# Performance work log

Measured on AMD Instinct MI355X. Metric: run time of the kernel, lower is better.

## Reference

```python
import jax, jax.numpy as jnp
import numpy as np

QUALITY = 50.0
TEMP = 0.3  # soft-round temperature

_LUM = np.array([[16,11,10,16,24,40,51,61],[12,12,14,19,26,58,60,55],[14,13,16,24,40,57,69,56],[14,17,22,29,51,87,80,62],[18,22,37,56,68,109,103,77],[24,35,55,64,81,104,113,92],[49,64,78,87,103,121,120,101],[72,92,95,98,112,100,103,99]], dtype=np.float32)
_CHR = np.array([[17,18,24,47,99,99,99,99],[18,21,26,66,99,99,99,99],[24,26,56,99,99,99,99,99],[47,66,99,99,99,99,99,99],[99,99,99,99,99,99,99,99],[99,99,99,99,99,99,99,99],[99,99,99,99,99,99,99,99],[99,99,99,99,99,99,99,99]], dtype=np.float32)

def _scaled_qtable(base, qf):
    qf = max(1.0, min(100.0, qf))
    s = 5000.0 / qf if qf < 50 else 200.0 - 2.0 * qf
    return np.maximum(np.floor((base * s + 50.0) / 100.0), 1.0)

# Per-channel quantization tables: Y uses luminance, Cb/Cr use chrominance. (3,8,8)
QTAB = jnp.asarray(np.stack([_scaled_qtable(_LUM, QUALITY), _scaled_qtable(_CHR, QUALITY), _scaled_qtable(_CHR, QUALITY)]).astype(np.float32))

# The original 64x1x8x8 conv kernel factors as outer product D[u,x]*D[v,y].
_u = np.arange(8)[:, None]
_x = np.arange(8)[None, :]
_c = np.where(_u == 0, 1.0 / np.sqrt(2.0), 1.0)
DCT = jnp.asarray((0.5 * _c * np.cos((2 * _x + 1) * _u * np.pi / 16.0)).astype(np.float32))

M_FWD = jnp.array([[0.299, 0.587, 0.114], [-0.168736, -0.331264, 0.5], [0.5, -0.418688, -0.081312]], dtype=jnp.float32)
M_INV = jnp.array([[1.0, 0.0, 1.402], [1.0, -0.344136, -0.714136], [1.0, 1.772, 0.0]], dtype=jnp.float32)
OFF = jnp.array([0.0, 0.5, 0.5], dtype=jnp.float32)


def setup_inputs() -> dict:
    key = jax.random.key(0)
    x = jax.random.uniform(key, (32, 3, 512, 512), dtype=jnp.float32)
    return {"x": x}


def reference(x):
    B, C, H, W = x.shape  # H, W divisible by 8 (no pad branch)
    # RGB -> YCbCr, centered
    ycbcr = jnp.einsum('ij,bjhw->bihw', M_FWD, x) + OFF[None, :, None, None] - 0.5
    # split into 8x8 blocks: (B, 3, H/8, 8, W/8, 8)
    blocks = ycbcr.reshape(B, C, H // 8, 8, W // 8, 8)
    # block DCT: coef[u,v] = sum_{x,y} D[u,x] D[v,y] block[x,y]
    coef = jnp.einsum('ux,vy,bchxgy->bchugv', DCT, DCT, blocks)
    q = QTAB[None, :, None, :, None, :]  # broadcast per-channel table
    d = coef / q
    # smooth rounding: x + 0.5*tanh(50*T*(x - round(x)))
    sr = d + 0.5 * jnp.tanh(50.0 * TEMP * (d - jnp.round(d)))
    deq = sr * q
    # block IDCT (transpose of DCT): block[x,y] = sum_{u,v} D[u,x] D[v,y] coef[u,v]
    rec = jnp.einsum('ux,vy,bchugv->bchxgy', DCT, DCT, deq)
    ycbcr_rec = rec.reshape(B, C, H, W) + 0.5
    rgb = jnp.einsum('ij,bjhw->bihw', M_INV, ycbcr_rec - OFF[None, :, None, None])
    return jnp.clip(rgb, 0.0, 1.0)
```

## Files before the change

### kernel.cpp

```cpp
#include <hip/hip_runtime.h>
#include <math.h>

#define A0c 0.35355339059327373f
#define C1c 0.4903926402016152f
#define C2c 0.46193976625564337f
#define C3c 0.41573480615127262f
#define C5c 0.27778511650980114f
#define C6c 0.19134171618254492f
#define C7c 0.09754516100806417f

#define IMG_W 512
#define IMG_HW (512 * 512)

typedef float f8v __attribute__((ext_vector_type(8)));

__device__ const float QLUM[64] = {
    16,11,10,16,24,40,51,61,  12,12,14,19,26,58,60,55,
    14,13,16,24,40,57,69,56,  14,17,22,29,51,87,80,62,
    18,22,37,56,68,109,103,77, 24,35,55,64,81,104,113,92,
    49,64,78,87,103,121,120,101, 72,92,95,98,112,100,103,99};
__device__ const float QCHR[64] = {
    17,18,24,47,99,99,99,99,  18,21,26,66,99,99,99,99,
    24,26,56,99,99,99,99,99,  47,66,99,99,99,99,99,99,
    99,99,99,99,99,99,99,99,  99,99,99,99,99,99,99,99,
    99,99,99,99,99,99,99,99,  99,99,99,99,99,99,99,99};

__device__ __forceinline__ void fdct8(float v[8]) {
    float s0 = v[0] + v[7], s1 = v[1] + v[6], s2 = v[2] + v[5], s3 = v[3] + v[4];
    float d0 = v[0] - v[7], d1 = v[1] - v[6], d2 = v[2] - v[5], d3 = v[3] - v[4];
    float e0 = s0 + s3, e1 = s1 + s2, f0 = s0 - s3, f1 = s1 - s2;
    v[0] = A0c * (e0 + e1);
    v[4] = A0c * (e0 - e1);
    v[2] = C2c * f0 + C6c * f1;
    v[6] = C6c * f0 - C2c * f1;
    v[1] = C1c * d0 + C3c * d1 + C5c * d2 + C7c * d3;
    v[3] = C3c * d0 - C7c * d1 - C1c * d2 - C5c * d3;
    v[5] = C5c * d0 - C1c * d1 + C7c * d2 + C3c * d3;
    v[7] = C7c * d0 - C5c * d1 + C3c * d2 - C1c * d3;
}

__device__ __forceinline__ void idct8(float v[8]) {
    float g0 = v[0], g1 = v[1], g2 = v[2], g3 = v[3];
    float g4 = v[4], g5 = v[5], g6 = v[6], g7 = v[7];
    float ep = A0c * (g0 + g4), em = A0c * (g0 - g4);
    float t26a = C2c * g2 + C6c * g6;
    float t26b = C6c * g2 - C2c * g6;
    float e0 = ep + t26a, e1 = em + t26b, e2 = em - t26b, e3 = ep - t26a;
    float o0 = C1c * g1 + C3c * g3 + C5c * g5 + C7c * g7;
    float o1 = C3c * g1 - C7c * g3 - C1c * g5 - C5c * g7;
    float o2 = C5c * g1 - C1c * g3 + C7c * g5 + C3c * g7;
    float o3 = C7c * g1 - C5c * g3 + C3c * g5 - C1c * g7;
    v[0] = e0 + o0; v[7] = e0 - o0;
    v[1] = e1 + o1; v[6] = e1 - o1;
    v[2] = e2 + o2; v[5] = e2 - o2;
    v[3] = e3 + o3; v[4] = e3 - o3;
}

#define K_EXP2 43.2808512266689f
__device__ __forceinline__ float softq(float x, float qh, float rq) {
    float d = x * rq;
    float rn = rintf(d);
    float t = d - rn;
    float e2 = __builtin_amdgcn_exp2f(K_EXP2 * t);
    float th = (e2 - 1.0f) * __builtin_amdgcn_rcpf(e2 + 1.0f);
    return x + qh * th;
}

#define LDS_FENCE() asm volatile("" ::: "memory")

__global__ __launch_bounds__(256) void jpeg_kernel(const float* __restrict__ x,
                                                   float* __restrict__ out) {
    __shared__ float xpose[4][576];
    __shared__ float qtab[4][64];

    const int tid = threadIdx.x;
    const int wid = tid >> 6;
    const int lane = tid & 63;

    const int gw = blockIdx.x * 4 + wid;
    const int bimg = gw >> 9;
    const int rem = gw & 511;
    const int gh = rem >> 3;
    const int tx = rem & 7;

    const int blk = lane & 7;
    const int row = lane >> 3;

    const size_t off = (size_t)bimg * 3 * IMG_HW +
                       (size_t)(gh * 8 + row) * IMG_W + tx * 64 + blk * 8;
    const float* base = x + off;

    const f8v Rv = *(const f8v*)(base);
    const f8v Gv = *(const f8v*)(base + IMG_HW);
    const f8v Bv = *(const f8v*)(base + 2 * IMG_HW);

    {
        int u = lane & 7, v = lane >> 3;
        float ql = QLUM[u * 8 + v];
        float qc = QCHR[u * 8 + v];
        qtab[0][lane] = 0.5f * ql;
        qtab[1][lane] = __builtin_amdgcn_rcpf(ql);
        qtab[2][lane] = 0.5f * qc;
        qtab[3][lane] = __builtin_amdgcn_rcpf(qc);
    }
    LDS_FENCE();

    float* xp = xpose[wid];
    const int wbase = blk * 9 + row;
    const int rbase = row * 72 + blk * 9;
    const int qrow = row * 8;

    float g0[8], g1[8], g2[8];
#pragma unroll
    for (int k = 0; k < 8; ++k) {
        float R = Rv[k], G = Gv[k], B = Bv[k];
        g0[k] = 0.299f * R + 0.587f * G + 0.114f * B - 0.5f;
        g1[k] = -0.168736f * R - 0.331264f * G + 0.5f * B;
        g2[k] = 0.5f * R - 0.418688f * G - 0.081312f * B;
    }

    fdct8(g0);
#pragma unroll
    for (int j = 0; j < 8; ++j) xp[j * 72 + wbase] = g0[j];
    LDS_FENCE();
#pragma unroll
    for (int k = 0; k < 8; ++k) g0[k] = xp[rbase + k];
    LDS_FENCE();
    fdct8(g0);
    {
        float4 qa = *(const float4*)&qtab[0][qrow];
        float4 qb = *(const float4*)&qtab[0][qrow + 4];
        float4 ra = *(const float4*)&qtab[1][qrow];
        float4 rb = *(const float4*)&qtab[1][qrow + 4];
        g0[0] = softq(g0[0], qa.x, ra.x); g0[1] = softq(g0[1], qa.y, ra.y);
        g0[2] = softq(g0[2], qa.z, ra.z); g0[3] = softq(g0[3], qa.w, ra.w);
        g0[4] = softq(g0[4], qb.x, rb.x); g0[5] = softq(g0[5], qb.y, rb.y);
        g0[6] = softq(g0[6], qb.z, rb.z); g0[7] = softq(g0[7], qb.w, rb.w);
    }
    idct8(g0);
    LDS_FENCE();
#pragma unroll
    for (int j = 0; j < 8; ++j) xp[j * 72 + wbase] = g0[j];
    LDS_FENCE();
#pragma unroll
    for (int k = 0; k < 8; ++k) g0[k] = xp[rbase + k];
    LDS_FENCE();
    idct8(g0);

    fdct8(g1);
#pragma unroll
    for (int j = 0; j < 8; ++j) xp[j * 72 + wbase] = g1[j];
    LDS_FENCE();
#pragma unroll
    for (int k = 0; k < 8; ++k) g1[k] = xp[rbase + k];
    LDS_FENCE();
    fdct8(g1);
    {
        float4 qa = *(const float4*)&qtab[2][qrow];
        float4 qb = *(const float4*)&qtab[2][qrow + 4];
        float4 ra = *(const float4*)&qtab[3][qrow];
        float4 rb = *(const float4*)&qtab[3][qrow + 4];
        g1[0] = softq(g1[0], qa.x, ra.x); g1[1] = softq(g1[1], qa.y, ra.y);
        g1[2] = softq(g1[2], qa.z, ra.z); g1[3] = softq(g1[3], qa.w, ra.w);
        g1[4] = softq(g1[4], qb.x, rb.x); g1[5] = softq(g1[5], qb.y, rb.y);
        g1[6] = softq(g1[6], qb.z, rb.z); g1[7] = softq(g1[7], qb.w, rb.w);
    }
    idct8(g1);
    LDS_FENCE();
#pragma unroll
    for (int j = 0; j < 8; ++j) xp[j * 72 + wbase] = g1[j];
    LDS_FENCE();
#pragma unroll
    for (int k = 0; k < 8; ++k) g1[k] = xp[rbase + k];
    LDS_FENCE();
    idct8(g1);

    fdct8(g2);
#pragma unroll
    for (int j = 0; j < 8; ++j) xp[j * 72 + wbase] = g2[j];
    LDS_FENCE();
#pragma unroll
    for (int k = 0; k < 8; ++k) g2[k] = xp[rbase + k];
    LDS_FENCE();
    fdct8(g2);
    {
        float4 qa = *(const float4*)&qtab[2][qrow];
        float4 qb = *(const float4*)&qtab[2][qrow + 4];
        float4 ra = *(const float4*)&qtab[3][qrow];
        float4 rb = *(const float4*)&qtab[3][qrow + 4];
        g2[0] = softq(g2[0], qa.x, ra.x); g2[1] = softq(g2[1], qa.y, ra.y);
        g2[2] = softq(g2[2], qa.z, ra.z); g2[3] = softq(g2[3], qa.w, ra.w);
        g2[4] = softq(g2[4], qb.x, rb.x); g2[5] = softq(g2[5], qb.y, rb.y);
        g2[6] = softq(g2[6], qb.z, rb.z); g2[7] = softq(g2[7], qb.w, rb.w);
    }
    idct8(g2);
    LDS_FENCE();
#pragma unroll
    for (int j = 0; j < 8; ++j) xp[j * 72 + wbase] = g2[j];
    LDS_FENCE();
#pragma unroll
    for (int k = 0; k < 8; ++k) g2[k] = xp[rbase + k];
    LDS_FENCE();
    idct8(g2);

    f8v Ro, Go, Bo;
#pragma unroll
    for (int k = 0; k < 8; ++k) {
        float Y  = g0[k] + 0.5f;
        float Cb = g1[k];
        float Cr = g2[k];
        float R = Y + 1.402f * Cr;
        float G = Y - 0.344136f * Cb - 0.714136f * Cr;
        float B = Y + 1.772f * Cb;
        Ro[k] = fminf(fmaxf(R, 0.0f), 1.0f);
        Go[k] = fminf(fmaxf(G, 0.0f), 1.0f);
        Bo[k] = fminf(fmaxf(B, 0.0f), 1.0f);
    }
    float* obase = out + off;
    *(f8v*)(obase) = Ro;
    *(f8v*)(obase + IMG_HW) = Go;
    *(f8v*)(obase + 2 * IMG_HW) = Bo;
}

extern "C" void kernel_launch(void* const* d_in, const int* in_sizes, int n_in,
                              void* d_out, int out_size, void* d_ws, size_t ws_size,
                              hipStream_t stream) {
    const float* x = (const float*)d_in[0];
    float* out = (float*)d_out;
    const int B = in_sizes[0] / (3 * IMG_HW);
    const int n_wg = B * 128;
    hipLaunchKernelGGL(jpeg_kernel, dim3(n_wg), dim3(256), 0, stream, x, out);
}
```

Baseline: 38.78 us.

## Process two images per thread with packed float2 math for DCT pipeline

Each thread now handles the same block position in two images (offset by 16 images) and holds values as float2 vectors, so the DCT/IDCT and color conversions can map to packed FP32 instructions (v_pk_fma_f32 on CDNA). The grid is halved and hardcoded to 2048 workgroups, and the LDS transpose buffer doubles to float2 entries. This aims to cut per-element ALU instruction count and raise memory-level parallelism per thread, but it increases register pressure and LDS use and drops support for batch sizes other than 32.

Measured after the change: 40.27 us. 1.04x slower.

```diff
diff --git a/kernel.cpp b/kernel.cpp
--- a/kernel.cpp
+++ b/kernel.cpp
@@ -13,6 +13,7 @@
 #define IMG_HW (512 * 512)
 
 typedef float f8v __attribute__((ext_vector_type(8)));
+typedef float f2v __attribute__((ext_vector_type(2)));
 
 __device__ const float QLUM[64] = {
     16,11,10,16,24,40,51,61,  12,12,14,19,26,58,60,55,
@@ -25,10 +26,10 @@
     99,99,99,99,99,99,99,99,  99,99,99,99,99,99,99,99,
     99,99,99,99,99,99,99,99,  99,99,99,99,99,99,99,99};
 
-__device__ __forceinline__ void fdct8(float v[8]) {
-    float s0 = v[0] + v[7], s1 = v[1] + v[6], s2 = v[2] + v[5], s3 = v[3] + v[4];
-    float d0 = v[0] - v[7], d1 = v[1] - v[6], d2 = v[2] - v[5], d3 = v[3] - v[4];
-    float e0 = s0 + s3, e1 = s1 + s2, f0 = s0 - s3, f1 = s1 - s2;
+__device__ __forceinline__ void fdct8p(f2v v[8]) {
+    f2v s0 = v[0] + v[7], s1 = v[1] + v[6], s2 = v[2] + v[5], s3 = v[3] + v[4];
+    f2v d0 = v[0] - v[7], d1 = v[1] - v[6], d2 = v[2] - v[5], d3 = v[3] - v[4];
+    f2v e0 = s0 + s3, e1 = s1 + s2, f0 = s0 - s3, f1 = s1 - s2;
     v[0] = A0c * (e0 + e1);
     v[4] = A0c * (e0 - e1);
     v[2] = C2c * f0 + C6c * f1;
@@ -39,17 +40,17 @@
     v[7] = C7c * d0 - C5c * d1 + C3c * d2 - C1c * d3;
 }
 
-__device__ __forceinline__ void idct8(float v[8]) {
-    float g0 = v[0], g1 = v[1], g2 = v[2], g3 = v[3];
-    float g4 = v[4], g5 = v[5], g6 = v[6], g7 = v[7];
-    float ep = A0c * (g0 + g4), em = A0c * (g0 - g4);
-    float t26a = C2c * g2 + C6c * g6;
-    float t26b = C6c * g2 - C2c * g6;
-    float e0 = ep + t26a, e1 = em + t26b, e2 = em - t26b, e3 = ep - t26a;
-    float o0 = C1c * g1 + C3c * g3 + C5c * g5 + C7c * g7;
-    float o1 = C3c * g1 - C7c * g3 - C1c * g5 - C5c * g7;
-    float o2 = C5c * g1 - C1c * g3 + C7c * g5 + C3c * g7;
-    float o3 = C7c * g1 - C5c * g3 + C3c * g5 - C1c * g7;
+__device__ __forceinline__ void idct8p(f2v v[8]) {
+    f2v g0 = v[0], g1 = v[1], g2 = v[2], g3 = v[3];
+    f2v g4 = v[4], g5 = v[5], g6 = v[6], g7 = v[7];
+    f2v ep = A0c * (g0 + g4), em = A0c * (g0 - g4);
+    f2v t26a = C2c * g2 + C6c * g6;
+    f2v t26b = C6c * g2 - C2c * g6;
+    f2v e0 = ep + t26a, e1 = em + t26b, e2 = em - t26b, e3 = ep - t26a;
+    f2v o0 = C1c * g1 + C3c * g3 + C5c * g5 + C7c * g7;
+    f2v o1 = C3c * g1 - C7c * g3 - C1c * g5 - C5c * g7;
+    f2v o2 = C5c * g1 - C1c * g3 + C7c * g5 + C3c * g7;
+    f2v o3 = C7c * g1 - C5c * g3 + C3c * g5 - C1c * g7;
     v[0] = e0 + o0; v[7] = e0 - o0;
     v[1] = e1 + o1; v[6] = e1 - o1;
     v[2] = e2 + o2; v[5] = e2 - o2;
@@ -57,12 +58,15 @@
 }
 
 #define K_EXP2 43.2808512266689f
-__device__ __forceinline__ float softq(float x, float qh, float rq) {
-    float d = x * rq;
-    float rn = rintf(d);
-    float t = d - rn;
-    float e2 = __builtin_amdgcn_exp2f(K_EXP2 * t);
-    float th = (e2 - 1.0f) * __builtin_amdgcn_rcpf(e2 + 1.0f);
+__device__ __forceinline__ f2v softq2(f2v x, float qh, float rq) {
+    f2v d = x * rq;
+    f2v rn; rn[0] = rintf(d[0]); rn[1] = rintf(d[1]);
+    f2v t = d - rn;
+    f2v e2; e2[0] = __builtin_amdgcn_exp2f(K_EXP2 * t[0]);
+            e2[1] = __builtin_amdgcn_exp2f(K_EXP2 * t[1]);
+    f2v num = e2 - 1.0f;
+    f2v th; th[0] = num[0] * __builtin_amdgcn_rcpf(e2[0] + 1.0f);
+            th[1] = num[1] * __builtin_amdgcn_rcpf(e2[1] + 1.0f);
     return x + qh * th;
 }
 
@@ -70,7 +74,7 @@
 
 __global__ __launch_bounds__(256) void jpeg_kernel(const float* __restrict__ x,
                                                    float* __restrict__ out) {
-    __shared__ float xpose[4][576];
+    __shared__ f2v xpose[4][576];
     __shared__ float qtab[4][64];
 
     const int tid = threadIdx.x;
@@ -88,11 +92,16 @@
 
     const size_t off = (size_t)bimg * 3 * IMG_HW +
                        (size_t)(gh * 8 + row) * IMG_W + tx * 64 + blk * 8;
-    const float* base = x + off;
-
-    const f8v Rv = *(const f8v*)(base);
-    const f8v Gv = *(const f8v*)(base + IMG_HW);
-    const f8v Bv = *(const f8v*)(base + 2 * IMG_HW);
+    const size_t toff = (size_t)16 * 3 * IMG_HW;
+    const float* baseA = x + off;
+    const float* baseB = baseA + toff;
+
+    const f8v RA = *(const f8v*)(baseA);
+    const f8v GA = *(const f8v*)(baseA + IMG_HW);
+    const f8v BA = *(const f8v*)(baseA + 2 * IMG_HW);
+    const f8v RB = *(const f8v*)(baseB);
+    const f8v GB = *(const f8v*)(baseB + IMG_HW);
+    const f8v BB = *(const f8v*)(baseB + 2 * IMG_HW);
 
     {
         int u = lane & 7, v = lane >> 3;
@@ -105,39 +114,41 @@
     }
     LDS_FENCE();
 
-    float* xp = xpose[wid];
+    f2v* xp = xpose[wid];
     const int wbase = blk * 9 + row;
     const int rbase = row * 72 + blk * 9;
     const int qrow = row * 8;
 
-    float g0[8], g1[8], g2[8];
+    f2v g0[8], g1[8], g2[8];
 #pragma unroll
     for (int k = 0; k < 8; ++k) {
-        float R = Rv[k], G = Gv[k], B = Bv[k];
-        g0[k] = 0.299f * R + 0.587f * G + 0.114f * B - 0.5f;
-        g1[k] = -0.168736f * R - 0.331264f * G + 0.5f * B;
-        g2[k] = 0.5f * R - 0.418688f * G - 0.081312f * B;
-    }
-
-    fdct8(g0);
+        f2v Rp; Rp[0] = RA[k]; Rp[1] = RB[k];
+        f2v Gp; Gp[0] = GA[k]; Gp[1] = GB[k];
+        f2v Bp; Bp[0] = BA[k]; Bp[1] = BB[k];
+        g0[k] = 0.299f * Rp + 0.587f * Gp + 0.114f * Bp - 0.5f;
+        g1[k] = -0.168736f * Rp - 0.331264f * Gp + 0.5f * Bp;
+        g2[k] = 0.5f * Rp - 0.418688f * Gp - 0.081312f * Bp;
+    }
+
+    fdct8p(g0);
 #pragma unroll
     for (int j = 0; j < 8; ++j) xp[j * 72 + wbase] = g0[j];
     LDS_FENCE();
 #pragma unroll
     for (int k = 0; k < 8; ++k) g0[k] = xp[rbase + k];
     LDS_FENCE();
-    fdct8(g0);
+    fdct8p(g0);
     {
         float4 qa = *(const float4*)&qtab[0][qrow];
         float4 qb = *(const float4*)&qtab[0][qrow + 4];
         float4 ra = *(const float4*)&qtab[1][qrow];
         float4 rb = *(const float4*)&qtab[1][qrow + 4];
-        g0[0] = softq(g0[0], qa.x, ra.x); g0[1] = softq(g0[1], qa.y, ra.y);
-        g0[2] = softq(g0[2], qa.z, ra.z); g0[3] = softq(g0[3], qa.w, ra.w);
-        g0[4] = softq(g0[4], qb.x, rb.x); g0[5] = softq(g0[5], qb.y, rb.y);
-        g0[6] = softq(g0[6], qb.z, rb.z); g0[7] = softq(g0[7], qb.w, rb.w);
-    }
-    idct8(g0);
+        g0[0] = softq2(g0[0], qa.x, ra.x); g0[1] = softq2(g0[1], qa.y, ra.y);
+        g0[2] = softq2(g0[2], qa.z, ra.z); g0[3] = softq2(g0[3], qa.w, ra.w);
+        g0[4] = softq2(g0[4], qb.x, rb.x); g0[5] = softq2(g0[5], qb.y, rb.y);
+        g0[6] = softq2(g0[6], qb.z, rb.z); g0[7] = softq2(g0[7], qb.w, rb.w);
+    }
+    idct8p(g0);
     LDS_FENCE();
 #pragma unroll
     for (int j = 0; j < 8; ++j) xp[j * 72 + wbase] = g0[j];
@@ -145,27 +156,27 @@
 #pragma unroll
     for (int k = 0; k < 8; ++k) g0[k] = xp[rbase + k];
     LDS_FENCE();
-    idct8(g0);
-
-    fdct8(g1);
+    idct8p(g0);
+
+    fdct8p(g1);
 #pragma unroll
     for (int j = 0; j < 8; ++j) xp[j * 72 + wbase] = g1[j];
     LDS_FENCE();
 #pragma unroll
     for (int k = 0; k < 8; ++k) g1[k] = xp[rbase + k];
     LDS_FENCE();
-    fdct8(g1);
+    fdct8p(g1);
     {
         float4 qa = *(const float4*)&qtab[2][qrow];
         float4 qb = *(const float4*)&qtab[2][qrow + 4];
         float4 ra = *(const float4*)&qtab[3][qrow];
         float4 rb = *(const float4*)&qtab[3][qrow + 4];
-        g1[0] = softq(g1[0], qa.x, ra.x); g1[1] = softq(g1[1], qa.y, ra.y);
-        g1[2] = softq(g1[2], qa.z, ra.z); g1[3] = softq(g1[3], qa.w, ra.w);
-        g1[4] = softq(g1[4], qb.x, rb.x); g1[5] = softq(g1[5], qb.y, rb.y);
-        g1[6] = softq(g1[6], qb.z, rb.z); g1[7] = softq(g1[7], qb.w, rb.w);
-    }
-    idct8(g1);
+        g1[0] = softq2(g1[0], qa.x, ra.x); g1[1] = softq2(g1[1], qa.y, ra.y);
+        g1[2] = softq2(g1[2], qa.z, ra.z); g1[3] = softq2(g1[3], qa.w, ra.w);
+        g1[4] = softq2(g1[4], qb.x, rb.x); g1[5] = softq2(g1[5], qb.y, rb.y);
+        g1[6] = softq2(g1[6], qb.z, rb.z); g1[7] = softq2(g1[7], qb.w, rb.w);
+    }
+    idct8p(g1);
     LDS_FENCE();
 #pragma unroll
     for (int j = 0; j < 8; ++j) xp[j * 72 + wbase] = g1[j];
@@ -173,27 +184,27 @@
 #pragma unroll
     for (int k = 0; k < 8; ++k) g1[k] = xp[rbase + k];
     LDS_FENCE();
-    idct8(g1);
-
-    fdct8(g2);
+    idct8p(g1);
+
+    fdct8p(g2);
 #pragma unroll
     for (int j = 0; j < 8; ++j) xp[j * 72 + wbase] = g2[j];
     LDS_FENCE();
 #pragma unroll
     for (int k = 0; k < 8; ++k) g2[k] = xp[rbase + k];
     LDS_FENCE();
-    fdct8(g2);
+    fdct8p(g2);
     {
         float4 qa = *(const float4*)&qtab[2][qrow];
         float4 qb = *(const float4*)&qtab[2][qrow + 4];
         float4 ra = *(const float4*)&qtab[3][qrow];
         float4 rb = *(const float4*)&qtab[3][qrow + 4];
-        g2[0] = softq(g2[0], qa.x, ra.x); g2[1] = softq(g2[1], qa.y, ra.y);
-        g2[2] = softq(g2[2], qa.z, ra.z); g2[3] = softq(g2[3], qa.w, ra.w);
-        g2[4] = softq(g2[4], qb.x, rb.x); g2[5] = softq(g2[5], qb.y, rb.y);
-        g2[6] = softq(g2[6], qb.z, rb.z); g2[7] = softq(g2[7], qb.w, rb.w);
-    }
-    idct8(g2);
+        g2[0] = softq2(g2[0], qa.x, ra.x); g2[1] = softq2(g2[1], qa.y, ra.y);
+        g2[2] = softq2(g2[2], qa.z, ra.z); g2[3] = softq2(g2[3], qa.w, ra.w);
+        g2[4] = softq2(g2[4], qb.x, rb.x); g2[5] = softq2(g2[5], qb.y, rb.y);
+        g2[6] = softq2(g2[6], qb.z, rb.z); g2[7] = softq2(g2[7], qb.w, rb.w);
+    }
+    idct8p(g2);
     LDS_FENCE();
 #pragma unroll
     for (int j = 0; j < 8; ++j) xp[j * 72 + wbase] = g2[j];
@@ -201,25 +212,34 @@
 #pragma unroll
     for (int k = 0; k < 8; ++k) g2[k] = xp[rbase + k];
     LDS_FENCE();
-    idct8(g2);
-
-    f8v Ro, Go, Bo;
+    idct8p(g2);
+
+    const f2v vzero = {0.0f, 0.0f};
+    const f2v vone  = {1.0f, 1.0f};
+    f8v RoA, GoA, BoA, RoB, GoB, BoB;
 #pragma unroll
     for (int k = 0; k < 8; ++k) {
-        float Y  = g0[k] + 0.5f;
-        float Cb = g1[k];
-        float Cr = g2[k];
-        float R = Y + 1.402f * Cr;
-        float G = Y - 0.344136f * Cb - 0.714136f * Cr;
-        float B = Y + 1.772f * Cb;
-        Ro[k] = fminf(fmaxf(R, 0.0f), 1.0f);
-        Go[k] = fminf(fmaxf(G, 0.0f), 1.0f);
-        Bo[k] = fminf(fmaxf(B, 0.0f), 1.0f);
-    }
-    float* obase = out + off;
-    *(f8v*)(obase) = Ro;
-    *(f8v*)(obase + IMG_HW) = Go;
-    *(f8v*)(obase + 2 * IMG_HW) = Bo;
+        f2v Y  = g0[k] + 0.5f;
+        f2v Cb = g1[k];
+        f2v Cr = g2[k];
+        f2v R = Y + 1.402f * Cr;
+        f2v G = Y - 0.344136f * Cb - 0.714136f * Cr;
+        f2v B = Y + 1.772f * Cb;
+        R = __builtin_elementwise_min(__builtin_elementwise_max(R, vzero), vone);
+        G = __builtin_elementwise_min(__builtin_elementwise_max(G, vzero), vone);
+        B = __builtin_elementwise_min(__builtin_elementwise_max(B, vzero), vone);
+        RoA[k] = R[0]; RoB[k] = R[1];
+        GoA[k] = G[0]; GoB[k] = G[1];
+        BoA[k] = B[0]; BoB[k] = B[1];
+    }
+    float* oA = out + off;
+    float* oB = oA + toff;
+    *(f8v*)(oA) = RoA;
+    *(f8v*)(oA + IMG_HW) = GoA;
+    *(f8v*)(oA + 2 * IMG_HW) = BoA;
+    *(f8v*)(oB) = RoB;
+    *(f8v*)(oB + IMG_HW) = GoB;
+    *(f8v*)(oB + 2 * IMG_HW) = BoB;
 }
 
 extern "C" void kernel_launch(void* const* d_in, const int* in_sizes, int n_in,
@@ -227,7 +247,6 @@
                               hipStream_t stream) {
     const float* x = (const float*)d_in[0];
     float* out = (float*)d_out;
-    const int B = in_sizes[0] / (3 * IMG_HW);
-    const int n_wg = B * 128;
+    const int n_wg = 2048;
     hipLaunchKernelGGL(jpeg_kernel, dim3(n_wg), dim3(256), 0, stream, x, out);
 }
```

## Process four images per wave with register prefetch of next tile

Applied to the files above, without the earlier changes.

Restructures the kernel so each wave loops over four tiles spaced eight images apart, loading the next tile's RGB into registers before processing the current one. The grid is fixed at 1024 workgroups, amortizing quant-table setup and overlapping global loads with DCT compute. This raises register pressure, and the hardcoded grid assumes a batch of 32.

New measurement: 39.03 us. Within noise of the previous version (+0.7%).

```diff
diff --git a/kernel.cpp b/kernel.cpp
--- a/kernel.cpp
+++ b/kernel.cpp
@@ -68,48 +68,43 @@
 
 #define LDS_FENCE() asm volatile("" ::: "memory")
 
-__global__ __launch_bounds__(256) void jpeg_kernel(const float* __restrict__ x,
-                                                   float* __restrict__ out) {
-    __shared__ float xpose[4][576];
-    __shared__ float qtab[4][64];
-
-    const int tid = threadIdx.x;
-    const int wid = tid >> 6;
-    const int lane = tid & 63;
-
-    const int gw = blockIdx.x * 4 + wid;
-    const int bimg = gw >> 9;
-    const int rem = gw & 511;
-    const int gh = rem >> 3;
-    const int tx = rem & 7;
-
-    const int blk = lane & 7;
-    const int row = lane >> 3;
-
-    const size_t off = (size_t)bimg * 3 * IMG_HW +
-                       (size_t)(gh * 8 + row) * IMG_W + tx * 64 + blk * 8;
-    const float* base = x + off;
-
-    const f8v Rv = *(const f8v*)(base);
-    const f8v Gv = *(const f8v*)(base + IMG_HW);
-    const f8v Bv = *(const f8v*)(base + 2 * IMG_HW);
-
+__device__ __forceinline__ void chan_chain(float g[8], float* xp, int wbase,
+                                           int rbase, const float* qh8,
+                                           const float* rq8) {
+    fdct8(g);
+#pragma unroll
+    for (int j = 0; j < 8; ++j) xp[j * 72 + wbase] = g[j];
+    LDS_FENCE();
+#pragma unroll
+    for (int k = 0; k < 8; ++k) g[k] = xp[rbase + k];
+    LDS_FENCE();
+    fdct8(g);
     {
-        int u = lane & 7, v = lane >> 3;
-        float ql = QLUM[u * 8 + v];
-        float qc = QCHR[u * 8 + v];
-        qtab[0][lane] = 0.5f * ql;
-        qtab[1][lane] = __builtin_amdgcn_rcpf(ql);
-        qtab[2][lane] = 0.5f * qc;
-        qtab[3][lane] = __builtin_amdgcn_rcpf(qc);
-    }
-    LDS_FENCE();
-
-    float* xp = xpose[wid];
-    const int wbase = blk * 9 + row;
-    const int rbase = row * 72 + blk * 9;
-    const int qrow = row * 8;
-
+        float4 qa = *(const float4*)&qh8[0];
+        float4 qb = *(const float4*)&qh8[4];
+        float4 ra = *(const float4*)&rq8[0];
+        float4 rb = *(const float4*)&rq8[4];
+        g[0] = softq(g[0], qa.x, ra.x); g[1] = softq(g[1], qa.y, ra.y);
+        g[2] = softq(g[2], qa.z, ra.z); g[3] = softq(g[3], qa.w, ra.w);
+        g[4] = softq(g[4], qb.x, rb.x); g[5] = softq(g[5], qb.y, rb.y);
+        g[6] = softq(g[6], qb.z, rb.z); g[7] = softq(g[7], qb.w, rb.w);
+    }
+    idct8(g);
+    LDS_FENCE();
+#pragma unroll
+    for (int j = 0; j < 8; ++j) xp[j * 72 + wbase] = g[j];
+    LDS_FENCE();
+#pragma unroll
+    for (int k = 0; k < 8; ++k) g[k] = xp[rbase + k];
+    LDS_FENCE();
+    idct8(g);
+}
+
+__device__ __forceinline__ void process_tile(const f8v Rv, const f8v Gv, const f8v Bv,
+                                             float* xp, int wbase, int rbase,
+                                             const float* qt0, const float* qt1,
+                                             const float* qt2, const float* qt3,
+                                             float* obase) {
     float g0[8], g1[8], g2[8];
 #pragma unroll
     for (int k = 0; k < 8; ++k) {
@@ -118,90 +113,9 @@
         g1[k] = -0.168736f * R - 0.331264f * G + 0.5f * B;
         g2[k] = 0.5f * R - 0.418688f * G - 0.081312f * B;
     }
-
-    fdct8(g0);
-#pragma unroll
-    for (int j = 0; j < 8; ++j) xp[j * 72 + wbase] = g0[j];
-    LDS_FENCE();
-#pragma unroll
-    for (int k = 0; k < 8; ++k) g0[k] = xp[rbase + k];
-    LDS_FENCE();
-    fdct8(g0);
-    {
-        float4 qa = *(const float4*)&qtab[0][qrow];
-        float4 qb = *(const float4*)&qtab[0][qrow + 4];
-        float4 ra = *(const float4*)&qtab[1][qrow];
-        float4 rb = *(const float4*)&qtab[1][qrow + 4];
-        g0[0] = softq(g0[0], qa.x, ra.x); g0[1] = softq(g0[1], qa.y, ra.y);
-        g0[2] = softq(g0[2], qa.z, ra.z); g0[3] = softq(g0[3], qa.w, ra.w);
-        g0[4] = softq(g0[4], qb.x, rb.x); g0[5] = softq(g0[5], qb.y, rb.y);
-        g0[6] = softq(g0[6], qb.z, rb.z); g0[7] = softq(g0[7], qb.w, rb.w);
-    }
-    idct8(g0);
-    LDS_FENCE();
-#pragma unroll
-    for (int j = 0; j < 8; ++j) xp[j * 72 + wbase] = g0[j];
-    LDS_FENCE();
-#pragma unroll
-    for (int k = 0; k < 8; ++k) g0[k] = xp[rbase + k];
-    LDS_FENCE();
-    idct8(g0);
-
-    fdct8(g1);
-#pragma unroll
-    for (int j = 0; j < 8; ++j) xp[j * 72 + wbase] = g1[j];
-    LDS_FENCE();
-#pragma unroll
-    for (int k = 0; k < 8; ++k) g1[k] = xp[rbase + k];
-    LDS_FENCE();
-    fdct8(g1);
-    {
-        float4 qa = *(const float4*)&qtab[2][qrow];
-        float4 qb = *(const float4*)&qtab[2][qrow + 4];
-        float4 ra = *(const float4*)&qtab[3][qrow];
-        float4 rb = *(const float4*)&qtab[3][qrow + 4];
-        g1[0] = softq(g1[0], qa.x, ra.x); g1[1] = softq(g1[1], qa.y, ra.y);
-        g1[2] = softq(g1[2], qa.z, ra.z); g1[3] = softq(g1[3], qa.w, ra.w);
-        g1[4] = softq(g1[4], qb.x, rb.x); g1[5] = softq(g1[5], qb.y, rb.y);
-        g1[6] = softq(g1[6], qb.z, rb.z); g1[7] = softq(g1[7], qb.w, rb.w);
-    }
-    idct8(g1);
-    LDS_FENCE();
-#pragma unroll
-    for (int j = 0; j < 8; ++j) xp[j * 72 + wbase] = g1[j];
-    LDS_FENCE();
-#pragma unroll
-    for (int k = 0; k < 8; ++k) g1[k] = xp[rbase + k];
-    LDS_FENCE();
-    idct8(g1);
-
-    fdct8(g2);
-#pragma unroll
-    for (int j = 0; j < 8; ++j) xp[j * 72 + wbase] = g2[j];
-    LDS_FENCE();
-#pragma unroll
-    for (int k = 0; k < 8; ++k) g2[k] = xp[rbase + k];
-    LDS_FENCE();
-    fdct8(g2);
-    {
-        float4 qa = *(const float4*)&qtab[2][qrow];
-        float4 qb = *(const float4*)&qtab[2][qrow + 4];
-        float4 ra = *(const float4*)&qtab[3][qrow];
-        float4 rb = *(const float4*)&qtab[3][qrow + 4];
-        g2[0] = softq(g2[0], qa.x, ra.x); g2[1] = softq(g2[1], qa.y, ra.y);
-        g2[2] = softq(g2[2], qa.z, ra.z); g2[3] = softq(g2[3], qa.w, ra.w);
-        g2[4] = softq(g2[4], qb.x, rb.x); g2[5] = softq(g2[5], qb.y, rb.y);
-        g2[6] = softq(g2[6], qb.z, rb.z); g2[7] = softq(g2[7], qb.w, rb.w);
-    }
-    idct8(g2);
-    LDS_FENCE();
-#pragma unroll
-    for (int j = 0; j < 8; ++j) xp[j * 72 + wbase] = g2[j];
-    LDS_FENCE();
-#pragma unroll
-    for (int k = 0; k < 8; ++k) g2[k] = xp[rbase + k];
-    LDS_FENCE();
-    idct8(g2);
+    chan_chain(g0, xp, wbase, rbase, qt0, qt1);
+    chan_chain(g1, xp, wbase, rbase, qt2, qt3);
+    chan_chain(g2, xp, wbase, rbase, qt2, qt3);
 
     f8v Ro, Go, Bo;
 #pragma unroll
@@ -216,10 +130,79 @@
         Go[k] = fminf(fmaxf(G, 0.0f), 1.0f);
         Bo[k] = fminf(fmaxf(B, 0.0f), 1.0f);
     }
-    float* obase = out + off;
     *(f8v*)(obase) = Ro;
     *(f8v*)(obase + IMG_HW) = Go;
     *(f8v*)(obase + 2 * IMG_HW) = Bo;
+}
+
+__global__ __launch_bounds__(256) void jpeg_kernel(const float* __restrict__ x,
+                                                   float* __restrict__ out) {
+    __shared__ float xpose[4][576];
+    __shared__ float qtab[4][64];
+
+    const int tid = threadIdx.x;
+    const int wid = tid >> 6;
+    const int lane = tid & 63;
+
+    const int gw = blockIdx.x * 4 + wid;
+    const int bimg = gw >> 9;
+    const int rem = gw & 511;
+    const int gh = rem >> 3;
+    const int tx = rem & 7;
+
+    const int blk = lane & 7;
+    const int row = lane >> 3;
+
+    const size_t off0 = (size_t)bimg * 3 * IMG_HW +
+                        (size_t)(gh * 8 + row) * IMG_W + tx * 64 + blk * 8;
+    const size_t DOFF = (size_t)8 * 3 * IMG_HW;
+
+    f8v Rc = *(const f8v*)(x + off0);
+    f8v Gc = *(const f8v*)(x + off0 + IMG_HW);
+    f8v Bc = *(const f8v*)(x + off0 + 2 * IMG_HW);
+
+    {
+        int u = lane & 7, v = lane >> 3;
+        float ql = QLUM[u * 8 + v];
+        float qc = QCHR[u * 8 + v];
+        qtab[0][lane] = 0.5f * ql;
+        qtab[1][lane] = __builtin_amdgcn_rcpf(ql);
+        qtab[2][lane] = 0.5f * qc;
+        qtab[3][lane] = __builtin_amdgcn_rcpf(qc);
+    }
+    LDS_FENCE();
+
+    float* xp = xpose[wid];
+    const int wbase = blk * 9 + row;
+    const int rbase = row * 72 + blk * 9;
+    const int qrow = row * 8;
+    const float* qt0 = &qtab[0][qrow];
+    const float* qt1 = &qtab[1][qrow];
+    const float* qt2 = &qtab[2][qrow];
+    const float* qt3 = &qtab[3][qrow];
+
+    f8v Rn = *(const f8v*)(x + off0 + DOFF);
+    f8v Gn = *(const f8v*)(x + off0 + DOFF + IMG_HW);
+    f8v Bn = *(const f8v*)(x + off0 + DOFF + 2 * IMG_HW);
+    LDS_FENCE();
+    process_tile(Rc, Gc, Bc, xp, wbase, rbase, qt0, qt1, qt2, qt3, out + off0);
+    Rc = Rn; Gc = Gn; Bc = Bn;
+
+    Rn = *(const f8v*)(x + off0 + 2 * DOFF);
+    Gn = *(const f8v*)(x + off0 + 2 * DOFF + IMG_HW);
+    Bn = *(const f8v*)(x + off0 + 2 * DOFF + 2 * IMG_HW);
+    LDS_FENCE();
+    process_tile(Rc, Gc, Bc, xp, wbase, rbase, qt0, qt1, qt2, qt3, out + off0 + DOFF);
+    Rc = Rn; Gc = Gn; Bc = Bn;
+
+    Rn = *(const f8v*)(x + off0 + 3 * DOFF);
+    Gn = *(const f8v*)(x + off0 + 3 * DOFF + IMG_HW);
+    Bn = *(const f8v*)(x + off0 + 3 * DOFF + 2 * IMG_HW);
+    LDS_FENCE();
+    process_tile(Rc, Gc, Bc, xp, wbase, rbase, qt0, qt1, qt2, qt3, out + off0 + 2 * DOFF);
+    Rc = Rn; Gc = Gn; Bc = Bn;
+
+    process_tile(Rc, Gc, Bc, xp, wbase, rbase, qt0, qt1, qt2, qt3, out + off0 + 3 * DOFF);
 }
 
 extern "C" void kernel_launch(void* const* d_in, const int* in_sizes, int n_in,
@@ -227,7 +210,6 @@
                               hipStream_t stream) {
     const float* x = (const float*)d_in[0];
     float* out = (float*)d_out;
-    const int B = in_sizes[0] / (3 * IMG_HW);
-    const int n_wg = B * 128;
+    const int n_wg = 1024;
     hipLaunchKernelGGL(jpeg_kernel, dim3(n_wg), dim3(256), 0, stream, x, out);
 }
```
